# Kernel optimization log

Measured on AMD Instinct MI355X. Metric: run time of the kernel, lower is better.

Reference implementation:

```python
import jax, jax.numpy as jnp
import numpy as np
import math

B, S, D_MODEL, N_HEAD, D_HEAD, D_FFN = 1, 2048, 1024, 16, 64, 4096
EPS = 1e-6


def setup_inputs() -> dict:
    key = jax.random.key(0)
    ks = jax.random.split(key, 10)
    scale = 0.02
    x = jax.random.normal(ks[0], (B, S, D_MODEL), dtype=jnp.float32)
    # RoPE frequencies: freqs_cis[s, i] = exp(1j * s * theta_i), theta_i = 10000^{-2i/d_head}
    half = D_HEAD // 2
    inv_freq = 1.0 / (10000.0 ** (jnp.arange(0, half, dtype=jnp.float32) * 2.0 / D_HEAD))
    angles = jnp.arange(S, dtype=jnp.float32)[:, None] * inv_freq[None, :]  # [S, half]
    freqs_cos = jnp.cos(angles)
    freqs_sin = jnp.sin(angles)
    wq = jax.random.normal(ks[1], (D_MODEL, N_HEAD * D_HEAD), dtype=jnp.float32) * scale
    wk = jax.random.normal(ks[2], (D_MODEL, N_HEAD * D_HEAD), dtype=jnp.float32) * scale
    wv = jax.random.normal(ks[3], (D_MODEL, N_HEAD * D_HEAD), dtype=jnp.float32) * scale
    wo = jax.random.normal(ks[4], (N_HEAD * D_HEAD, D_MODEL), dtype=jnp.float32) * scale
    w1 = jax.random.normal(ks[5], (D_MODEL, D_FFN), dtype=jnp.float32) * scale
    w2 = jax.random.normal(ks[6], (D_FFN, D_MODEL), dtype=jnp.float32) * scale
    w3 = jax.random.normal(ks[7], (D_MODEL, D_FFN), dtype=jnp.float32) * scale
    attn_norm_w = jnp.ones((D_MODEL,), dtype=jnp.float32)
    ffn_norm_w = jnp.ones((D_MODEL,), dtype=jnp.float32)
    return {"x": x, "freqs_cos": freqs_cos, "freqs_sin": freqs_sin,
            "wq": wq, "wk": wk, "wv": wv, "wo": wo,
            "w1": w1, "w2": w2, "w3": w3,
            "attn_norm_w": attn_norm_w, "ffn_norm_w": ffn_norm_w}


def _rmsnorm(x, w):
    xf = x.astype(jnp.float32)
    inv = jax.lax.rsqrt(jnp.mean(xf * xf, axis=-1, keepdims=True) + EPS)
    return (xf * inv).astype(x.dtype) * w


def _rope(t, cos, sin):
    # t: [B, S, H, D]; treat last dim as interleaved (even, odd) complex pairs
    b, s, h, d = t.shape
    tr = t.astype(jnp.float32).reshape(b, s, h, d // 2, 2)
    te, to = tr[..., 0], tr[..., 1]
    c = cos[None, :, None, :]
    sn = sin[None, :, None, :]
    out = jnp.stack([te * c - to * sn, te * sn + to * c], axis=-1)
    return out.reshape(b, s, h, d).astype(t.dtype)


def reference(x, freqs_cos, freqs_sin, wq, wk, wv, wo, w1, w2, w3, attn_norm_w, ffn_norm_w):
    bsz, seqlen, _ = x.shape
    # --- attention sub-block ---
    hin = _rmsnorm(x, attn_norm_w)
    q = (hin @ wq).reshape(bsz, seqlen, N_HEAD, D_HEAD)
    k = (hin @ wk).reshape(bsz, seqlen, N_HEAD, D_HEAD)
    v = (hin @ wv).reshape(bsz, seqlen, N_HEAD, D_HEAD)
    q = _rope(q, freqs_cos, freqs_sin)
    k = _rope(k, freqs_cos, freqs_sin)
    # [B, H, S, S] scores, softmax in fp32 (no causal mask in original)
    scores = jnp.einsum('bqhd,bkhd->bhqk', q, k) / math.sqrt(D_HEAD)
    probs = jax.nn.softmax(scores.astype(jnp.float32), axis=-1).astype(q.dtype)
    attn = jnp.einsum('bhqk,bkhd->bqhd', probs, v).reshape(bsz, seqlen, N_HEAD * D_HEAD)
    h = x + attn @ wo
    # --- SwiGLU FFN sub-block ---
    f = _rmsnorm(h, ffn_norm_w)
    ffn = (jax.nn.silu(f @ w1) * (f @ w3)) @ w2
    return h + ffn
```

## Files before the change

kernel.cpp:

```cpp
#include <hip/hip_runtime.h>
#include <stdint.h>
#include <stddef.h>

using bf16x8 = __attribute__((ext_vector_type(8))) __bf16;
using f32x4  = __attribute__((ext_vector_type(4))) float;
using f32x16 = __attribute__((ext_vector_type(16))) float;

__device__ __forceinline__ float bf2f(unsigned short u) {
  union { unsigned int i; float f; } v; v.i = ((unsigned int)u) << 16; return v.f;
}
__device__ __forceinline__ unsigned short f2bf(float f) {
  union { float f; unsigned int i; } v; v.f = f;
  unsigned int r = v.i + 0x7fffu + ((v.i >> 16) & 1u);
  return (unsigned short)(r >> 16);
}
__device__ __forceinline__ unsigned short f2bf_trunc(float f) {
  union { float f; unsigned int i; } v; v.f = f;
  return (unsigned short)(v.i >> 16);
}
__device__ __forceinline__ void async16(const void* g, void* l) {
  __builtin_amdgcn_global_load_lds(
      (const __attribute__((address_space(1))) unsigned int*)g,
      (__attribute__((address_space(3))) unsigned int*)l, 16, 0, 0);
}

#define S_LEN 2048
#define DMODEL 1024
#define NHEAD 16
#define DHEAD 64
#define DFFN 4096

struct TAll {
  const float *wq, *wk, *wv, *wo, *w1, *w3, *w2;
  unsigned short *qkvT, *woT, *w13I, *w2T;
};
__global__ __launch_bounds__(256) void transpose_all_k(TAll j) {
  __shared__ unsigned short tile[32][33];
  const int tx = threadIdx.x & 31;
  const int ty = threadIdx.x >> 5;
  const unsigned u = blockIdx.x;

  const float* in;
  unsigned short* out;
  int bc, br, inC, outR, rs, rb;
  if (u < 4096) {
    int z = u >> 10;
    bc = (u & 31) * 32; br = ((u >> 5) & 31) * 32;
    in = z == 0 ? j.wq : z == 1 ? j.wk : z == 2 ? j.wv : j.wo;
    out = z == 3 ? j.woT : j.qkvT + (size_t)z * 1048576;
    inC = 1024; outR = 1024; rs = 32; rb = 0;
  } else if (u < 12288) {
    unsigned v = u - 4096;
    int z = v >> 12;
    bc = (v & 127) * 32; br = ((v >> 7) & 31) * 32;
    in = z ? j.w3 : j.w1;
    out = j.w13I;
    inC = 4096; outR = 1024; rs = 64; rb = z * 32;
  } else {
    unsigned v = u - 12288;
    bc = (v & 31) * 32; br = (v >> 5) * 32;
    in = j.w2; out = j.w2T;
    inC = 1024; outR = 4096; rs = 32; rb = 0;
  }
#pragma unroll
  for (int i = 0; i < 4; ++i)
    tile[ty + i * 8][tx] = f2bf(in[(size_t)(br + ty + i * 8) * inC + bc + tx]);
  __syncthreads();
#pragma unroll
  for (int i = 0; i < 4; ++i) {
    int c = bc + ty + i * 8;
    int dest = (c >> 5) * rs + rb + (c & 31);
    out[(size_t)dest * outR + br + tx] = tile[tx][ty + i * 8];
  }
}

__global__ __launch_bounds__(256) void vtrans_k(
    const unsigned short* __restrict__ QKV, unsigned short* __restrict__ VtG) {
  __shared__ unsigned short tile[32][33];
  const int tx = threadIdx.x & 31;
  const int ty = threadIdx.x >> 5;
  const int bc = blockIdx.x * 32;
  const int br = blockIdx.y * 32;
#pragma unroll
  for (int i = 0; i < 4; ++i)
    tile[ty + i * 8][tx] = QKV[(size_t)(br + ty + i * 8) * 3072 + 2048 + bc + tx];
  __syncthreads();
#pragma unroll
  for (int i = 0; i < 4; ++i)
    VtG[(size_t)(bc + ty + i * 8) * 2048 + br + tx] = tile[tx][ty + i * 8];
}

__global__ __launch_bounds__(256) void rmsnorm_k(
    const float* __restrict__ X, const float* __restrict__ W,
    unsigned short* __restrict__ Y) {
  const int row = blockIdx.x;
  const int t = threadIdx.x;
  const int lane = t & 63, w = t >> 6;
  const float* x = X + (size_t)row * DMODEL;
  float xs[4];
  float s = 0.f;
#pragma unroll
  for (int i = 0; i < 4; ++i) {
    xs[i] = x[t * 4 + i];
    s += xs[i] * xs[i];
  }
#pragma unroll
  for (int m = 1; m < 64; m <<= 1) s += __shfl_xor(s, m, 64);
  __shared__ float red[4];
  if (lane == 0) red[w] = s;
  __syncthreads();
  float tot = red[0] + red[1] + red[2] + red[3];
  float inv = rsqrtf(tot * (1.0f / DMODEL) + 1e-6f);
#pragma unroll
  for (int i = 0; i < 4; ++i)
    Y[(size_t)row * DMODEL + t * 4 + i] = f2bf(xs[i] * inv * W[t * 4 + i]);
}

__global__ __launch_bounds__(256) void fused_res_norm_k(
    const float* __restrict__ P0, const float* __restrict__ P1,
    const float* __restrict__ R, const float* __restrict__ W,
    float* __restrict__ Hres, unsigned short* __restrict__ Hin) {
  const int row = blockIdx.x;
  const int t = threadIdx.x;
  const int lane = t & 63, w = t >> 6;
  const size_t base = (size_t)row * DMODEL;
  float hs[4];
  float s = 0.f;
#pragma unroll
  for (int i = 0; i < 4; ++i) {
    int c = t * 4 + i;
    float h = P0[base + c] + P1[base + c] + R[base + c];
    hs[i] = h;
    Hres[base + c] = h;
    s += h * h;
  }
#pragma unroll
  for (int m = 1; m < 64; m <<= 1) s += __shfl_xor(s, m, 64);
  __shared__ float red[4];
  if (lane == 0) red[w] = s;
  __syncthreads();
  float tot = red[0] + red[1] + red[2] + red[3];
  float inv = rsqrtf(tot * (1.0f / DMODEL) + 1e-6f);
#pragma unroll
  for (int i = 0; i < 4; ++i)
    Hin[base + t * 4 + i] = f2bf(hs[i] * inv * W[t * 4 + i]);
}

__global__ __launch_bounds__(256) void gemm_bt0_k(
    const unsigned short* __restrict__ A,
    const unsigned short* __restrict__ BT,
    unsigned short* __restrict__ C,
    int K, int N) {
  __shared__ unsigned short As[128 * 64];
  __shared__ unsigned short Bs[128 * 64];
  const int t = threadIdx.x;
  const int lane = t & 63;
  const int w = t >> 6;
  const int qr = (w >> 1) * 64, qc = (w & 1) * 64;
  const int l31 = lane & 31, half = lane >> 5;
  const int m0 = blockIdx.y * 128, n0 = blockIdx.x * 128;

  f32x16 acc[2][2] = {};

  for (int k0 = 0; k0 < K; k0 += 64) {
    __syncthreads();
#pragma unroll
    for (int p = 0; p < 4; ++p) {
      int off = p * 2048 + t * 8;
      int r = off >> 6;
      int sc = (((off >> 3) & 7) ^ (r & 7)) * 8;
      async16(A + (size_t)(m0 + r) * K + (k0 + sc), &As[off]);
      async16(BT + (size_t)(n0 + r) * K + (k0 + sc), &Bs[off]);
    }
    __syncthreads();
#pragma unroll
    for (int ks = 0; ks < 4; ++ks) {
      const int ch = ((ks * 2 + half) ^ (l31 & 7)) * 8;
      bf16x8 a0 = *(const bf16x8*)&As[(qr + l31) * 64 + ch];
      bf16x8 a1 = *(const bf16x8*)&As[(qr + 32 + l31) * 64 + ch];
      bf16x8 b0 = *(const bf16x8*)&Bs[(qc + l31) * 64 + ch];
      bf16x8 b1 = *(const bf16x8*)&Bs[(qc + 32 + l31) * 64 + ch];
      acc[0][0] = __builtin_amdgcn_mfma_f32_32x32x16_bf16(a0, b0, acc[0][0], 0, 0, 0);
      acc[0][1] = __builtin_amdgcn_mfma_f32_32x32x16_bf16(a0, b1, acc[0][1], 0, 0, 0);
      acc[1][0] = __builtin_amdgcn_mfma_f32_32x32x16_bf16(a1, b0, acc[1][0], 0, 0, 0);
      acc[1][1] = __builtin_amdgcn_mfma_f32_32x32x16_bf16(a1, b1, acc[1][1], 0, 0, 0);
    }
  }

#pragma unroll
  for (int rt = 0; rt < 2; ++rt)
#pragma unroll
    for (int ct = 0; ct < 2; ++ct)
#pragma unroll
      for (int reg = 0; reg < 16; ++reg) {
        int rr = m0 + qr + rt * 32 + (reg & 3) + 8 * (reg >> 2) + 4 * half;
        int cc = n0 + qc + ct * 32 + l31;
        C[(size_t)rr * N + cc] = f2bf(acc[rt][ct][reg]);
      }
}

__global__ __launch_bounds__(256) void rope_k(
    unsigned short* __restrict__ QKV,
    const float* __restrict__ cosp,
    const float* __restrict__ sinp) {
  int idx = blockIdx.x * 256 + threadIdx.x;
  int s = idx >> 9;
  int rem = idx & 511;
  int h = rem >> 5;
  int i = rem & 31;
  float c = cosp[s * 32 + i];
  float sn = sinp[s * 32 + i];
  size_t off = (size_t)s * 3072 + h * 64 + 2 * i;
  {
    float e = bf2f(QKV[off]), o = bf2f(QKV[off + 1]);
    QKV[off] = f2bf(e * c - o * sn);
    QKV[off + 1] = f2bf(e * sn + o * c);
  }
  {
    float e = bf2f(QKV[off + 1024]), o = bf2f(QKV[off + 1025]);
    QKV[off + 1024] = f2bf((e * c - o * sn) * 0.125f);
    QKV[off + 1025] = f2bf((e * sn + o * c) * 0.125f);
  }
}

__global__ __launch_bounds__(256) void gemm_gated_k(
    const unsigned short* __restrict__ A,
    const unsigned short* __restrict__ BT,
    unsigned short* __restrict__ C) {
  __shared__ unsigned short As[256 * 64];
  __shared__ unsigned short Bs[128 * 64];
  const int t = threadIdx.x;
  const int lane = t & 63;
  const int w = t >> 6;
  const int wm = w >> 1, wn = w & 1;
  const int l31 = lane & 31, half = lane >> 5;
  const int m0 = blockIdx.y * 256, n0 = blockIdx.x * 128;
  const int K = 1024;

  f32x16 acc[4][2] = {};

  for (int k0 = 0; k0 < K; k0 += 64) {
    __syncthreads();
#pragma unroll
    for (int p = 0; p < 8; ++p) {
      int off = p * 2048 + t * 8;
      int r = off >> 6;
      int sc = (((off >> 3) & 7) ^ (r & 7)) * 8;
      async16(A + (size_t)(m0 + r) * K + (k0 + sc), &As[off]);
    }
#pragma unroll
    for (int p = 0; p < 4; ++p) {
      int off = p * 2048 + t * 8;
      int r = off >> 6;
      int sc = (((off >> 3) & 7) ^ (r & 7)) * 8;
      async16(BT + (size_t)(n0 + r) * K + (k0 + sc), &Bs[off]);
    }
    __syncthreads();
#pragma unroll
    for (int ks = 0; ks < 4; ++ks) {
      const int ch = ((ks * 2 + half) ^ (l31 & 7)) * 8;
      bf16x8 b0 = *(const bf16x8*)&Bs[(wn * 64 + l31) * 64 + ch];
      bf16x8 b1 = *(const bf16x8*)&Bs[(wn * 64 + 32 + l31) * 64 + ch];
#pragma unroll
      for (int mt = 0; mt < 4; ++mt) {
        bf16x8 a = *(const bf16x8*)&As[(wm * 128 + mt * 32 + l31) * 64 + ch];
        acc[mt][0] = __builtin_amdgcn_mfma_f32_32x32x16_bf16(a, b0, acc[mt][0], 0, 0, 0);
        acc[mt][1] = __builtin_amdgcn_mfma_f32_32x32x16_bf16(a, b1, acc[mt][1], 0, 0, 0);
      }
    }
  }

  const int cc = ((n0 + wn * 64) >> 1) + l31;
#pragma unroll
  for (int mt = 0; mt < 4; ++mt)
#pragma unroll
    for (int reg = 0; reg < 16; ++reg) {
      int rr = m0 + wm * 128 + mt * 32 + (reg & 3) + 8 * (reg >> 2) + 4 * half;
      float g1 = acc[mt][0][reg];
      float g3 = acc[mt][1][reg];
      float f = g1 / (1.f + __expf(-g1)) * g3;
      C[(size_t)rr * 4096 + cc] = f2bf(f);
    }
}

struct PtrPair { float* p0; float* p1; };

__global__ __launch_bounds__(256) void gemm_bt_sk(
    const unsigned short* __restrict__ A, int lda,
    const unsigned short* __restrict__ BT,
    PtrPair parts, int Kc, int Ktot, int N) {
  __shared__ unsigned short As[64 * 64];
  __shared__ unsigned short Bs[128 * 64];
  const int t = threadIdx.x;
  const int lane = t & 63;
  const int w = t >> 6;
  const int qr = (w >> 1) * 32, qc = (w & 1) * 64;
  const int l31 = lane & 31, half = lane >> 5;
  const int m0 = blockIdx.y * 64, n0 = blockIdx.x * 128;
  const int kb = blockIdx.z * Kc;

  f32x16 acc[2] = {};

  for (int k0 = 0; k0 < Kc; k0 += 64) {
    __syncthreads();
#pragma unroll
    for (int p = 0; p < 2; ++p) {
      int off = p * 2048 + t * 8;
      int r = off >> 6;
      int sc = (((off >> 3) & 7) ^ (r & 7)) * 8;
      async16(A + (size_t)(m0 + r) * lda + (kb + k0 + sc), &As[off]);
    }
#pragma unroll
    for (int p = 0; p < 4; ++p) {
      int off = p * 2048 + t * 8;
      int r = off >> 6;
      int sc = (((off >> 3) & 7) ^ (r & 7)) * 8;
      async16(BT + (size_t)(n0 + r) * Ktot + (kb + k0 + sc), &Bs[off]);
    }
    __syncthreads();
#pragma unroll
    for (int ks = 0; ks < 4; ++ks) {
      const int ch = ((ks * 2 + half) ^ (l31 & 7)) * 8;
      bf16x8 a0 = *(const bf16x8*)&As[(qr + l31) * 64 + ch];
      bf16x8 b0 = *(const bf16x8*)&Bs[(qc + l31) * 64 + ch];
      bf16x8 b1 = *(const bf16x8*)&Bs[(qc + 32 + l31) * 64 + ch];
      acc[0] = __builtin_amdgcn_mfma_f32_32x32x16_bf16(a0, b0, acc[0], 0, 0, 0);
      acc[1] = __builtin_amdgcn_mfma_f32_32x32x16_bf16(a0, b1, acc[1], 0, 0, 0);
    }
  }

  float* C = blockIdx.z ? parts.p1 : parts.p0;
#pragma unroll
  for (int ct = 0; ct < 2; ++ct)
#pragma unroll
    for (int reg = 0; reg < 16; ++reg) {
      int rr = m0 + qr + (reg & 3) + 8 * (reg >> 2) + 4 * half;
      int cc = n0 + qc + ct * 32 + l31;
      C[(size_t)rr * N + cc] = acc[ct][reg];
    }
}

__global__ __launch_bounds__(256) void reduce2_k(
    const float4* __restrict__ P0, const float4* __restrict__ P1,
    const float4* __restrict__ R, float4* __restrict__ Out, int nvec) {
  int i = blockIdx.x * 256 + threadIdx.x;
  if (i >= nvec) return;
  float4 a = P0[i], b = P1[i], r = R[i];
  float4 o;
  o.x = a.x + b.x + r.x;
  o.y = a.y + b.y + r.y;
  o.z = a.z + b.z + r.z;
  o.w = a.w + b.w + r.w;
  Out[i] = o;
}

#define VPAD 132
__device__ __forceinline__ int swz(int row, int col) { return col ^ ((row & 7) * 8); }

__global__ __launch_bounds__(256) void attn_k(
    const unsigned short* __restrict__ QKV,
    const unsigned short* __restrict__ VtG,
    float* __restrict__ O0, float* __restrict__ O1,
    float* __restrict__ L) {
  const int h = blockIdx.y;
  const int qb = blockIdx.x;
  const int z = blockIdx.z;
  const int t = threadIdx.x;
  const int lane = t & 63;
  const int w = t >> 6;
  const int row16 = lane & 15, quad = lane >> 4;
  const int q0 = qb * 64 + w * 16;
  const int kbase = z * 1024;

  __shared__ unsigned short Ks[128 * 64];
  __shared__ unsigned short Vt[64 * 128];
  __shared__ unsigned short Ps[4][16 * VPAD];

  const unsigned short* Qp = QKV;
  const unsigned short* Kp = QKV + 1024;
  const unsigned short* Vg = VtG + (size_t)h * 64 * 2048;

  bf16x8 aq[2];
#pragma unroll
  for (int kk = 0; kk < 2; ++kk)
    aq[kk] = *(const bf16x8*)(Qp + (size_t)(q0 + row16) * 3072 + h * 64 + kk * 32 + quad * 8);

  f32x4 o[4] = {};
  float l_r[4] = {0.f, 0.f, 0.f, 0.f};

  bf16x8 kreg[4], vreg[4];
#pragma unroll
  for (int p = 0; p < 4; ++p) {
    int off = p * 2048 + t * 8;
    int r = off >> 6, c = off & 63;
    kreg[p] = *(const bf16x8*)(Kp + (size_t)(kbase + r) * 3072 + h * 64 + c);
    int d = off >> 7, key = off & 127;
    vreg[p] = *(const bf16x8*)(Vg + (size_t)d * 2048 + kbase + key);
  }

  for (int kb = kbase; kb < kbase + 1024; kb += 128) {
    __syncthreads();
#pragma unroll
    for (int p = 0; p < 4; ++p) {
      int off = p * 2048 + t * 8;
      int r = off >> 6, c = off & 63;
      *(bf16x8*)&Ks[r * 64 + swz(r, c)] = kreg[p];
      int d = off >> 7, key = off & 127;
      *(bf16x8*)&Vt[d * 128 + swz(d, key)] = vreg[p];
    }
    __syncthreads();
    if (kb + 128 < kbase + 1024) {
      int kb2 = kb + 128;
#pragma unroll
      for (int p = 0; p < 4; ++p) {
        int off = p * 2048 + t * 8;
        int r = off >> 6, c = off & 63;
        kreg[p] = *(const bf16x8*)(Kp + (size_t)(kb2 + r) * 3072 + h * 64 + c);
        int d = off >> 7, key = off & 127;
        vreg[p] = *(const bf16x8*)(Vg + (size_t)d * 2048 + kb2 + key);
      }
    }

    f32x4 sc[8];
#pragma unroll
    for (int tj = 0; tj < 8; ++tj) {
      int kr = tj * 16 + row16;
      bf16x8 b0 = *(const bf16x8*)&Ks[kr * 64 + swz(kr, quad * 8)];
      bf16x8 b1 = *(const bf16x8*)&Ks[kr * 64 + swz(kr, 32 + quad * 8)];
      f32x4 z4 = {};
      z4 = __builtin_amdgcn_mfma_f32_16x16x32_bf16(aq[0], b0, z4, 0, 0, 0);
      z4 = __builtin_amdgcn_mfma_f32_16x16x32_bf16(aq[1], b1, z4, 0, 0, 0);
      sc[tj] = z4;
    }

#pragma unroll
    for (int reg = 0; reg < 4; ++reg) {
      float ssum = 0.f;
#pragma unroll
      for (int tj = 0; tj < 8; ++tj) {
        float p = __expf(sc[tj][reg]);
        sc[tj][reg] = p;
        ssum += p;
      }
#pragma unroll
      for (int m = 1; m < 16; m <<= 1) ssum += __shfl_xor(ssum, m, 16);
      l_r[reg] += ssum;
    }

#pragma unroll
    for (int tj = 0; tj < 8; ++tj)
#pragma unroll
      for (int reg = 0; reg < 4; ++reg)
        Ps[w][(quad * 4 + reg) * VPAD + tj * 16 + row16] = f2bf_trunc(sc[tj][reg]);

    bf16x8 ap[4];
#pragma unroll
    for (int kk = 0; kk < 4; ++kk)
      ap[kk] = *(const bf16x8*)&Ps[w][row16 * VPAD + kk * 32 + quad * 8];
#pragma unroll
    for (int dt = 0; dt < 4; ++dt) {
      int dr = dt * 16 + row16;
#pragma unroll
      for (int kk = 0; kk < 4; ++kk) {
        bf16x8 bv = *(const bf16x8*)&Vt[dr * 128 + swz(dr, kk * 32 + quad * 8)];
        o[dt] = __builtin_amdgcn_mfma_f32_16x16x32_bf16(ap[kk], bv, o[dt], 0, 0, 0);
      }
    }
  }

  float* Op = z ? O1 : O0;
#pragma unroll
  for (int dt = 0; dt < 4; ++dt)
#pragma unroll
    for (int reg = 0; reg < 4; ++reg)
      Op[(size_t)(q0 + quad * 4 + reg) * DMODEL + h * 64 + dt * 16 + row16] = o[dt][reg];
  if (row16 == 0)
#pragma unroll
    for (int reg = 0; reg < 4; ++reg)
      L[(size_t)(h * 2 + z) * S_LEN + q0 + quad * 4 + reg] = l_r[reg];
}

__global__ __launch_bounds__(256) void attn_combine_k(
    const float4* __restrict__ O0, const float4* __restrict__ O1,
    const float* __restrict__ L, unsigned short* __restrict__ Attn) {
  int i = blockIdx.x * 256 + threadIdx.x;
  int e0 = i * 4;
  int s = e0 >> 10;
  int c = e0 & 1023;
  int h = c >> 6;
  float la = L[(size_t)(h * 2) * S_LEN + s];
  float lb = L[(size_t)(h * 2 + 1) * S_LEN + s];
  float inv = 1.f / (la + lb);
  float4 a = O0[i], b = O1[i];
  ushort4 r;
  r.x = f2bf((a.x + b.x) * inv);
  r.y = f2bf((a.y + b.y) * inv);
  r.z = f2bf((a.z + b.z) * inv);
  r.w = f2bf((a.w + b.w) * inv);
  *(ushort4*)(Attn + e0) = r;
}

extern "C" void kernel_launch(void* const* d_in, const int* in_sizes, int n_in,
                              void* d_out, int out_size, void* d_ws, size_t ws_size,
                              hipStream_t stream) {
  (void)in_sizes; (void)n_in; (void)out_size; (void)ws_size;
  const float* x    = (const float*)d_in[0];
  const float* fcos = (const float*)d_in[1];
  const float* fsin = (const float*)d_in[2];
  const float* wq   = (const float*)d_in[3];
  const float* wk   = (const float*)d_in[4];
  const float* wv   = (const float*)d_in[5];
  const float* wo   = (const float*)d_in[6];
  const float* w1   = (const float*)d_in[7];
  const float* w2   = (const float*)d_in[8];
  const float* w3   = (const float*)d_in[9];
  const float* anw  = (const float*)d_in[10];
  const float* fnw  = (const float*)d_in[11];
  float* out = (float*)d_out;
  char* ws = (char*)d_ws;

  unsigned short* WqkvT = (unsigned short*)(ws + 0);
  unsigned short* VtG   = (unsigned short*)(ws + 0);
  float*          Lbuf  = (float*)(ws + 4194304);
  unsigned short* WoT   = (unsigned short*)(ws + 6291456);
  unsigned short* QKV   = (unsigned short*)(ws + 8388608);
  unsigned short* Attn  = (unsigned short*)(ws + 20971520);
  float* Oa             = (float*)(ws + 25165824);
  float* Ob             = (float*)(ws + 37748736);
  float* P0a            = (float*)(ws + 8388608);
  float* P1a            = (float*)(ws + 25165824);
  unsigned short* F     = (unsigned short*)(ws + 0);
  float* P0b            = (float*)(ws + 16777216);
  float* P1b            = (float*)(ws + 25165824);
  unsigned short* Hin   = (unsigned short*)(ws + 33554432);
  float*          Hres  = (float*)        (ws + 37748736);
  unsigned short* W13I  = (unsigned short*)(ws + 46137344);
  unsigned short* W2T   = (unsigned short*)(ws + 62914560);

  transpose_all_k<<<16384, 256, 0, stream>>>(
      TAll{wq, wk, wv, wo, w1, w3, w2, WqkvT, WoT, W13I, W2T});

  rmsnorm_k<<<2048, 256, 0, stream>>>(x, anw, Hin);
  gemm_bt0_k<<<dim3(24, 16), 256, 0, stream>>>(Hin, WqkvT, QKV, 1024, 3072);
  rope_k<<<4096, 256, 0, stream>>>(QKV, fcos, fsin);
  vtrans_k<<<dim3(32, 64), 256, 0, stream>>>(QKV, VtG);
  attn_k<<<dim3(32, 16, 2), 256, 0, stream>>>(QKV, VtG, Oa, Ob, Lbuf);
  attn_combine_k<<<2048, 256, 0, stream>>>((const float4*)Oa, (const float4*)Ob, Lbuf, Attn);
  gemm_bt_sk<<<dim3(8, 32, 2), 256, 0, stream>>>(Attn, 1024, WoT, PtrPair{P0a, P1a}, 512, 1024, 1024);
  fused_res_norm_k<<<2048, 256, 0, stream>>>(P0a, P1a, x, fnw, Hres, Hin);

  gemm_gated_k<<<dim3(64, 8), 256, 0, stream>>>(Hin, W13I, F);
  gemm_bt_sk<<<dim3(8, 32, 2), 256, 0, stream>>>(F, 4096, W2T, PtrPair{P0b, P1b}, 2048, 4096, 1024);
  reduce2_k<<<2048, 256, 0, stream>>>((const float4*)P0b, (const float4*)P1b,
                                      (const float4*)Hres, (float4*)out, 524288);
}
```

Measured before the change: 317.3 us.

## Fuse prep and rope/vtrans launches, shrink QKV GEMM tile, split-K 4 for W2

Merges the weight transpose with the first RMSNorm into one launch, and RoPE with the V transpose into another, cutting launch count. The QKV projection GEMM now uses 64-row tiles so twice as many blocks fill the GPU. The down-projection GEMM moves from split-K 2 to split-K 4, writing four fp32 partials that a new reduce4 kernel sums with the residual. The extra partial buffers reuse workspace regions that held W13I after the gated GEMM; the costs are more partial-sum traffic and less reuse per GEMM tile.

```diff
diff --git a/kernel.cpp b/kernel.cpp
--- a/kernel.cpp
+++ b/kernel.cpp
@@ -30,90 +30,114 @@
 #define DHEAD 64
 #define DFFN 4096
 
-struct TAll {
+struct PrepArgs {
   const float *wq, *wk, *wv, *wo, *w1, *w3, *w2;
   unsigned short *qkvT, *woT, *w13I, *w2T;
+  const float *x, *anw;
+  unsigned short *Hin;
 };
-__global__ __launch_bounds__(256) void transpose_all_k(TAll j) {
-  __shared__ unsigned short tile[32][33];
-  const int tx = threadIdx.x & 31;
-  const int ty = threadIdx.x >> 5;
+__global__ __launch_bounds__(256) void prep_k(PrepArgs j) {
   const unsigned u = blockIdx.x;
-
-  const float* in;
-  unsigned short* out;
-  int bc, br, inC, outR, rs, rb;
+  if (u < 16384) {
+    __shared__ unsigned short tile[32][33];
+    const int tx = threadIdx.x & 31;
+    const int ty = threadIdx.x >> 5;
+    const float* in;
+    unsigned short* out;
+    int bc, br, inC, outR, rs, rb;
+    if (u < 4096) {
+      int z = u >> 10;
+      bc = (u & 31) * 32; br = ((u >> 5) & 31) * 32;
+      in = z == 0 ? j.wq : z == 1 ? j.wk : z == 2 ? j.wv : j.wo;
+      out = z == 3 ? j.woT : j.qkvT + (size_t)z * 1048576;
+      inC = 1024; outR = 1024; rs = 32; rb = 0;
+    } else if (u < 12288) {
+      unsigned v = u - 4096;
+      int z = v >> 12;
+      bc = (v & 127) * 32; br = ((v >> 7) & 31) * 32;
+      in = z ? j.w3 : j.w1;
+      out = j.w13I;
+      inC = 4096; outR = 1024; rs = 64; rb = z * 32;
+    } else {
+      unsigned v = u - 12288;
+      bc = (v & 31) * 32; br = (v >> 5) * 32;
+      in = j.w2; out = j.w2T;
+      inC = 1024; outR = 4096; rs = 32; rb = 0;
+    }
+#pragma unroll
+    for (int i = 0; i < 4; ++i)
+      tile[ty + i * 8][tx] = f2bf(in[(size_t)(br + ty + i * 8) * inC + bc + tx]);
+    __syncthreads();
+#pragma unroll
+    for (int i = 0; i < 4; ++i) {
+      int c = bc + ty + i * 8;
+      int dest = (c >> 5) * rs + rb + (c & 31);
+      out[(size_t)dest * outR + br + tx] = tile[tx][ty + i * 8];
+    }
+  } else {
+    const int row = u - 16384;
+    const int t = threadIdx.x;
+    const int lane = t & 63, w = t >> 6;
+    const float* x = j.x + (size_t)row * DMODEL;
+    float xs[4];
+    float s = 0.f;
+#pragma unroll
+    for (int i = 0; i < 4; ++i) {
+      xs[i] = x[t * 4 + i];
+      s += xs[i] * xs[i];
+    }
+#pragma unroll
+    for (int m = 1; m < 64; m <<= 1) s += __shfl_xor(s, m, 64);
+    __shared__ float red[4];
+    if (lane == 0) red[w] = s;
+    __syncthreads();
+    float tot = red[0] + red[1] + red[2] + red[3];
+    float inv = rsqrtf(tot * (1.0f / DMODEL) + 1e-6f);
+#pragma unroll
+    for (int i = 0; i < 4; ++i)
+      j.Hin[(size_t)row * DMODEL + t * 4 + i] = f2bf(xs[i] * inv * j.anw[t * 4 + i]);
+  }
+}
+
+__global__ __launch_bounds__(256) void rope_vtrans_k(
+    unsigned short* __restrict__ QKV,
+    const float* __restrict__ cosp, const float* __restrict__ sinp,
+    unsigned short* __restrict__ VtG) {
+  const unsigned u = blockIdx.x;
   if (u < 4096) {
-    int z = u >> 10;
-    bc = (u & 31) * 32; br = ((u >> 5) & 31) * 32;
-    in = z == 0 ? j.wq : z == 1 ? j.wk : z == 2 ? j.wv : j.wo;
-    out = z == 3 ? j.woT : j.qkvT + (size_t)z * 1048576;
-    inC = 1024; outR = 1024; rs = 32; rb = 0;
-  } else if (u < 12288) {
+    int idx = u * 256 + threadIdx.x;
+    int s = idx >> 9;
+    int rem = idx & 511;
+    int h = rem >> 5;
+    int i = rem & 31;
+    float c = cosp[s * 32 + i];
+    float sn = sinp[s * 32 + i];
+    size_t off = (size_t)s * 3072 + h * 64 + 2 * i;
+    {
+      float e = bf2f(QKV[off]), o = bf2f(QKV[off + 1]);
+      QKV[off] = f2bf(e * c - o * sn);
+      QKV[off + 1] = f2bf(e * sn + o * c);
+    }
+    {
+      float e = bf2f(QKV[off + 1024]), o = bf2f(QKV[off + 1025]);
+      QKV[off + 1024] = f2bf((e * c - o * sn) * 0.125f);
+      QKV[off + 1025] = f2bf((e * sn + o * c) * 0.125f);
+    }
+  } else {
+    __shared__ unsigned short tile[32][33];
     unsigned v = u - 4096;
-    int z = v >> 12;
-    bc = (v & 127) * 32; br = ((v >> 7) & 31) * 32;
-    in = z ? j.w3 : j.w1;
-    out = j.w13I;
-    inC = 4096; outR = 1024; rs = 64; rb = z * 32;
-  } else {
-    unsigned v = u - 12288;
-    bc = (v & 31) * 32; br = (v >> 5) * 32;
-    in = j.w2; out = j.w2T;
-    inC = 1024; outR = 4096; rs = 32; rb = 0;
-  }
-#pragma unroll
-  for (int i = 0; i < 4; ++i)
-    tile[ty + i * 8][tx] = f2bf(in[(size_t)(br + ty + i * 8) * inC + bc + tx]);
-  __syncthreads();
-#pragma unroll
-  for (int i = 0; i < 4; ++i) {
-    int c = bc + ty + i * 8;
-    int dest = (c >> 5) * rs + rb + (c & 31);
-    out[(size_t)dest * outR + br + tx] = tile[tx][ty + i * 8];
-  }
-}
-
-__global__ __launch_bounds__(256) void vtrans_k(
-    const unsigned short* __restrict__ QKV, unsigned short* __restrict__ VtG) {
-  __shared__ unsigned short tile[32][33];
-  const int tx = threadIdx.x & 31;
-  const int ty = threadIdx.x >> 5;
-  const int bc = blockIdx.x * 32;
-  const int br = blockIdx.y * 32;
-#pragma unroll
-  for (int i = 0; i < 4; ++i)
-    tile[ty + i * 8][tx] = QKV[(size_t)(br + ty + i * 8) * 3072 + 2048 + bc + tx];
-  __syncthreads();
-#pragma unroll
-  for (int i = 0; i < 4; ++i)
-    VtG[(size_t)(bc + ty + i * 8) * 2048 + br + tx] = tile[tx][ty + i * 8];
-}
-
-__global__ __launch_bounds__(256) void rmsnorm_k(
-    const float* __restrict__ X, const float* __restrict__ W,
-    unsigned short* __restrict__ Y) {
-  const int row = blockIdx.x;
-  const int t = threadIdx.x;
-  const int lane = t & 63, w = t >> 6;
-  const float* x = X + (size_t)row * DMODEL;
-  float xs[4];
-  float s = 0.f;
-#pragma unroll
-  for (int i = 0; i < 4; ++i) {
-    xs[i] = x[t * 4 + i];
-    s += xs[i] * xs[i];
-  }
-#pragma unroll
-  for (int m = 1; m < 64; m <<= 1) s += __shfl_xor(s, m, 64);
-  __shared__ float red[4];
-  if (lane == 0) red[w] = s;
-  __syncthreads();
-  float tot = red[0] + red[1] + red[2] + red[3];
-  float inv = rsqrtf(tot * (1.0f / DMODEL) + 1e-6f);
-#pragma unroll
-  for (int i = 0; i < 4; ++i)
-    Y[(size_t)row * DMODEL + t * 4 + i] = f2bf(xs[i] * inv * W[t * 4 + i]);
+    const int tx = threadIdx.x & 31;
+    const int ty = threadIdx.x >> 5;
+    const int bc = (v & 31) * 32;
+    const int br = (v >> 5) * 32;
+#pragma unroll
+    for (int i = 0; i < 4; ++i)
+      tile[ty + i * 8][tx] = QKV[(size_t)(br + ty + i * 8) * 3072 + 2048 + bc + tx];
+    __syncthreads();
+#pragma unroll
+    for (int i = 0; i < 4; ++i)
+      VtG[(size_t)(bc + ty + i * 8) * 2048 + br + tx] = tile[tx][ty + i * 8];
+  }
 }
 
 __global__ __launch_bounds__(256) void fused_res_norm_k(
@@ -146,30 +170,36 @@
     Hin[base + t * 4 + i] = f2bf(hs[i] * inv * W[t * 4 + i]);
 }
 
-__global__ __launch_bounds__(256) void gemm_bt0_k(
+__global__ __launch_bounds__(256) void gemm_bt64_k(
     const unsigned short* __restrict__ A,
     const unsigned short* __restrict__ BT,
     unsigned short* __restrict__ C,
     int K, int N) {
-  __shared__ unsigned short As[128 * 64];
+  __shared__ unsigned short As[64 * 64];
   __shared__ unsigned short Bs[128 * 64];
   const int t = threadIdx.x;
   const int lane = t & 63;
   const int w = t >> 6;
-  const int qr = (w >> 1) * 64, qc = (w & 1) * 64;
+  const int qr = (w >> 1) * 32, qc = (w & 1) * 64;
   const int l31 = lane & 31, half = lane >> 5;
-  const int m0 = blockIdx.y * 128, n0 = blockIdx.x * 128;
-
-  f32x16 acc[2][2] = {};
+  const int m0 = blockIdx.y * 64, n0 = blockIdx.x * 128;
+
+  f32x16 acc[2] = {};
 
   for (int k0 = 0; k0 < K; k0 += 64) {
     __syncthreads();
 #pragma unroll
-    for (int p = 0; p < 4; ++p) {
+    for (int p = 0; p < 2; ++p) {
       int off = p * 2048 + t * 8;
       int r = off >> 6;
       int sc = (((off >> 3) & 7) ^ (r & 7)) * 8;
       async16(A + (size_t)(m0 + r) * K + (k0 + sc), &As[off]);
+    }
+#pragma unroll
+    for (int p = 0; p < 4; ++p) {
+      int off = p * 2048 + t * 8;
+      int r = off >> 6;
+      int sc = (((off >> 3) & 7) ^ (r & 7)) * 8;
       async16(BT + (size_t)(n0 + r) * K + (k0 + sc), &Bs[off]);
     }
     __syncthreads();
@@ -177,50 +207,21 @@
     for (int ks = 0; ks < 4; ++ks) {
       const int ch = ((ks * 2 + half) ^ (l31 & 7)) * 8;
       bf16x8 a0 = *(const bf16x8*)&As[(qr + l31) * 64 + ch];
-      bf16x8 a1 = *(const bf16x8*)&As[(qr + 32 + l31) * 64 + ch];
       bf16x8 b0 = *(const bf16x8*)&Bs[(qc + l31) * 64 + ch];
       bf16x8 b1 = *(const bf16x8*)&Bs[(qc + 32 + l31) * 64 + ch];
-      acc[0][0] = __builtin_amdgcn_mfma_f32_32x32x16_bf16(a0, b0, acc[0][0], 0, 0, 0);
-      acc[0][1] = __builtin_amdgcn_mfma_f32_32x32x16_bf16(a0, b1, acc[0][1], 0, 0, 0);
-      acc[1][0] = __builtin_amdgcn_mfma_f32_32x32x16_bf16(a1, b0, acc[1][0], 0, 0, 0);
-      acc[1][1] = __builtin_amdgcn_mfma_f32_32x32x16_bf16(a1, b1, acc[1][1], 0, 0, 0);
-    }
-  }
-
-#pragma unroll
-  for (int rt = 0; rt < 2; ++rt)
-#pragma unroll
-    for (int ct = 0; ct < 2; ++ct)
-#pragma unroll
-      for (int reg = 0; reg < 16; ++reg) {
-        int rr = m0 + qr + rt * 32 + (reg & 3) + 8 * (reg >> 2) + 4 * half;
-        int cc = n0 + qc + ct * 32 + l31;
-        C[(size_t)rr * N + cc] = f2bf(acc[rt][ct][reg]);
-      }
-}
-
-__global__ __launch_bounds__(256) void rope_k(
-    unsigned short* __restrict__ QKV,
-    const float* __restrict__ cosp,
-    const float* __restrict__ sinp) {
-  int idx = blockIdx.x * 256 + threadIdx.x;
-  int s = idx >> 9;
-  int rem = idx & 511;
-  int h = rem >> 5;
-  int i = rem & 31;
-  float c = cosp[s * 32 + i];
-  float sn = sinp[s * 32 + i];
-  size_t off = (size_t)s * 3072 + h * 64 + 2 * i;
-  {
-    float e = bf2f(QKV[off]), o = bf2f(QKV[off + 1]);
-    QKV[off] = f2bf(e * c - o * sn);
-    QKV[off + 1] = f2bf(e * sn + o * c);
-  }
-  {
-    float e = bf2f(QKV[off + 1024]), o = bf2f(QKV[off + 1025]);
-    QKV[off + 1024] = f2bf((e * c - o * sn) * 0.125f);
-    QKV[off + 1025] = f2bf((e * sn + o * c) * 0.125f);
-  }
+      acc[0] = __builtin_amdgcn_mfma_f32_32x32x16_bf16(a0, b0, acc[0], 0, 0, 0);
+      acc[1] = __builtin_amdgcn_mfma_f32_32x32x16_bf16(a0, b1, acc[1], 0, 0, 0);
+    }
+  }
+
+#pragma unroll
+  for (int ct = 0; ct < 2; ++ct)
+#pragma unroll
+    for (int reg = 0; reg < 16; ++reg) {
+      int rr = m0 + qr + (reg & 3) + 8 * (reg >> 2) + 4 * half;
+      int cc = n0 + qc + ct * 32 + l31;
+      C[(size_t)rr * N + cc] = f2bf(acc[ct][reg]);
+    }
 }
 
 __global__ __launch_bounds__(256) void gemm_gated_k(
@@ -283,12 +284,13 @@
     }
 }
 
-struct PtrPair { float* p0; float* p1; };
-
+struct PtrQuad { float* p[4]; };
+
+template <int Z>
 __global__ __launch_bounds__(256) void gemm_bt_sk(
     const unsigned short* __restrict__ A, int lda,
     const unsigned short* __restrict__ BT,
-    PtrPair parts, int Kc, int Ktot, int N) {
+    PtrQuad parts, int Kc, int Ktot, int N) {
   __shared__ unsigned short As[64 * 64];
   __shared__ unsigned short Bs[128 * 64];
   const int t = threadIdx.x;
@@ -329,7 +331,7 @@
     }
   }
 
-  float* C = blockIdx.z ? parts.p1 : parts.p0;
+  float* C = parts.p[blockIdx.z & (Z - 1)];
 #pragma unroll
   for (int ct = 0; ct < 2; ++ct)
 #pragma unroll
@@ -351,6 +353,21 @@
   o.y = a.y + b.y + r.y;
   o.z = a.z + b.z + r.z;
   o.w = a.w + b.w + r.w;
+  Out[i] = o;
+}
+
+__global__ __launch_bounds__(256) void reduce4_k(
+    const float4* __restrict__ P0, const float4* __restrict__ P1,
+    const float4* __restrict__ P2, const float4* __restrict__ P3,
+    const float4* __restrict__ R, float4* __restrict__ Out, int nvec) {
+  int i = blockIdx.x * 256 + threadIdx.x;
+  if (i >= nvec) return;
+  float4 a = P0[i], b = P1[i], c = P2[i], d = P3[i], r = R[i];
+  float4 o;
+  o.x = (a.x + b.x) + (c.x + d.x) + r.x;
+  o.y = (a.y + b.y) + (c.y + d.y) + r.y;
+  o.z = (a.z + b.z) + (c.z + d.z) + r.z;
+  o.w = (a.w + b.w) + (c.w + d.w) + r.w;
   Out[i] = o;
 }
 
@@ -532,25 +549,28 @@
   unsigned short* F     = (unsigned short*)(ws + 0);
   float* P0b            = (float*)(ws + 16777216);
   float* P1b            = (float*)(ws + 25165824);
+  float* P2b            = (float*)(ws + 46137344);
+  float* P3b            = (float*)(ws + 54525952);
   unsigned short* Hin   = (unsigned short*)(ws + 33554432);
   float*          Hres  = (float*)        (ws + 37748736);
   unsigned short* W13I  = (unsigned short*)(ws + 46137344);
   unsigned short* W2T   = (unsigned short*)(ws + 62914560);
 
-  transpose_all_k<<<16384, 256, 0, stream>>>(
-      TAll{wq, wk, wv, wo, w1, w3, w2, WqkvT, WoT, W13I, W2T});
-
-  rmsnorm_k<<<2048, 256, 0, stream>>>(x, anw, Hin);
-  gemm_bt0_k<<<dim3(24, 16), 256, 0, stream>>>(Hin, WqkvT, QKV, 1024, 3072);
-  rope_k<<<4096, 256, 0, stream>>>(QKV, fcos, fsin);
-  vtrans_k<<<dim3(32, 64), 256, 0, stream>>>(QKV, VtG);
+  prep_k<<<18432, 256, 0, stream>>>(
+      PrepArgs{wq, wk, wv, wo, w1, w3, w2, WqkvT, WoT, W13I, W2T, x, anw, Hin});
+
+  gemm_bt64_k<<<dim3(24, 32), 256, 0, stream>>>(Hin, WqkvT, QKV, 1024, 3072);
+  rope_vtrans_k<<<6144, 256, 0, stream>>>(QKV, fcos, fsin, VtG);
   attn_k<<<dim3(32, 16, 2), 256, 0, stream>>>(QKV, VtG, Oa, Ob, Lbuf);
   attn_combine_k<<<2048, 256, 0, stream>>>((const float4*)Oa, (const float4*)Ob, Lbuf, Attn);
-  gemm_bt_sk<<<dim3(8, 32, 2), 256, 0, stream>>>(Attn, 1024, WoT, PtrPair{P0a, P1a}, 512, 1024, 1024);
+  gemm_bt_sk<2><<<dim3(8, 32, 2), 256, 0, stream>>>(
+      Attn, 1024, WoT, PtrQuad{{P0a, P1a, nullptr, nullptr}}, 512, 1024, 1024);
   fused_res_norm_k<<<2048, 256, 0, stream>>>(P0a, P1a, x, fnw, Hres, Hin);
 
   gemm_gated_k<<<dim3(64, 8), 256, 0, stream>>>(Hin, W13I, F);
-  gemm_bt_sk<<<dim3(8, 32, 2), 256, 0, stream>>>(F, 4096, W2T, PtrPair{P0b, P1b}, 2048, 4096, 1024);
-  reduce2_k<<<2048, 256, 0, stream>>>((const float4*)P0b, (const float4*)P1b,
+  gemm_bt_sk<4><<<dim3(8, 32, 4), 256, 0, stream>>>(
+      F, 4096, W2T, PtrQuad{{P0b, P1b, P2b, P3b}}, 1024, 4096, 1024);
+  reduce4_k<<<2048, 256, 0, stream>>>((const float4*)P0b, (const float4*)P1b,
+                                      (const float4*)P2b, (const float4*)P3b,
                                       (const float4*)Hres, (float4*)out, 524288);
 }
```

Result: no change. 322.0 us (+1.5%).
